# Performance work log

Hardware: AMD Instinct MI355X
Metric: run time of the kernel (lower is better)

Reference implementation:

```python
import jax, jax.numpy as jnp
import numpy as np

B, N, SEQ = 4, 1024, 512
FOUR = SEQ // 2 + 1           # 257, rfft output length
E = N * 32                    # edges from adjacency nonzeros
H1, C1 = 3, 10                # gat1: heads=3, out=10 (concat -> 30)
H2, C2 = 1, 1                 # gat2: heads=1, out=1
NEG_SLOPE = 0.2               # GATConv default negative_slope
PRE_L = 1


def setup_inputs() -> dict:
    ks = jax.random.split(jax.random.key(0), 14)
    occ = jax.random.normal(ks[0], (B, N, SEQ), dtype=jnp.float32)
    prc = jax.random.normal(ks[1], (B, N, SEQ), dtype=jnp.float32)
    # edge_index = adj_dense.nonzero().t(): indices in [0, N)
    edge_index = jax.random.randint(ks[2], (2, E), 0, N, dtype=jnp.int32)
    s = 0.3
    W1 = jax.random.normal(ks[3], (2, H1 * C1), dtype=jnp.float32) * s
    att_src1 = jax.random.normal(ks[4], (1, H1, C1), dtype=jnp.float32) * s
    att_dst1 = jax.random.normal(ks[5], (1, H1, C1), dtype=jnp.float32) * s
    b1 = jnp.zeros((H1 * C1,), dtype=jnp.float32)
    W2 = jax.random.normal(ks[6], (H1 * C1, H2 * C2), dtype=jnp.float32) * s
    att_src2 = jax.random.normal(ks[7], (1, H2, C2), dtype=jnp.float32) * s
    att_dst2 = jax.random.normal(ks[8], (1, H2, C2), dtype=jnp.float32) * s
    b2 = jnp.zeros((H2 * C2,), dtype=jnp.float32)
    dec_W = jax.random.normal(ks[9], (FOUR, PRE_L), dtype=jnp.float32) * (1.0 / np.sqrt(FOUR))
    dec_b = jnp.zeros((PRE_L,), dtype=jnp.float32)
    return {"occ": occ, "prc": prc, "edge_index": edge_index,
            "W1": W1, "att_src1": att_src1, "att_dst1": att_dst1, "b1": b1,
            "W2": W2, "att_src2": att_src2, "att_dst2": att_dst2, "b2": b2,
            "dec_W": dec_W, "dec_b": dec_b}


def gat_layer(x, src, dst, W, att_src, att_dst, bias, heads, ch):
    # x: [Nt, Fin]. PyG GATConv (concat=True, eval mode: no dropout).
    Nt = x.shape[0]
    h = (x @ W).reshape(Nt, heads, ch)                 # [Nt, H, C]
    a_src = jnp.sum(h * att_src, axis=-1)              # [Nt, H]
    a_dst = jnp.sum(h * att_dst, axis=-1)              # [Nt, H]
    e = jax.nn.leaky_relu(a_src[src] + a_dst[dst], NEG_SLOPE)  # [Ee, H]
    # segment softmax over destination nodes
    m = jax.ops.segment_max(e, dst, num_segments=Nt)   # [Nt, H]
    ex = jnp.exp(e - m[dst])
    denom = jax.ops.segment_sum(ex, dst, num_segments=Nt)
    alpha = ex / denom[dst]                            # [Ee, H]
    out = jax.ops.segment_sum(h[src] * alpha[..., None], dst, num_segments=Nt)
    return out.reshape(Nt, heads * ch) + bias


def reference(occ, prc, edge_index, W1, att_src1, att_dst1, b1,
              W2, att_src2, att_dst2, b2, dec_W, dec_b):
    # stack -> [B, N, SEQ, 2]; rfft over seq dim; keep real part
    x = jnp.stack([occ, prc], axis=-1)
    x = jnp.fft.rfft(x, axis=2).real                   # [B, N, FOUR, 2]
    x = x.reshape(-1, 2)                               # [Nt, 2], Nt = B*N*FOUR
    Nt = x.shape[0]
    # GATConv adds self-loops for every row of x (num_nodes = Nt)
    loops = jnp.arange(Nt, dtype=edge_index.dtype)
    src = jnp.concatenate([edge_index[0], loops])
    dst = jnp.concatenate([edge_index[1], loops])
    x = gat_layer(x, src, dst, W1, att_src1, att_dst1, b1, H1, C1)  # [Nt, 30]
    x = jax.nn.elu(x)
    x = gat_layer(x, src, dst, W2, att_src2, att_dst2, b2, H2, C2)  # [Nt, 1]
    # dropout is identity in eval mode
    x = x.reshape(B, N, FOUR)
    return x @ dec_W + dec_b                           # [B, N, PRE_L]
```

## Files before the change

### kernel.cpp

```cpp
#include <hip/hip_runtime.h>
#include <math.h>

constexpr int Bc    = 4;
constexpr int Nc    = 1024;
constexpr int SEQc  = 512;
constexpr int FOURc = 257;
constexpr int NROWS = Bc * Nc;
constexpr int NSMALL = 1024;
constexpr int F1c   = 30;
constexpr int CAP   = 128;
constexpr int XPAD  = 258;
constexpr float NEG_SLOPE = 0.2f;

#define DEVFN static __device__ __forceinline__

__global__ __launch_bounds__(256) void k_xf(
    const float* __restrict__ occ, const float* __restrict__ prc,
    float* __restrict__ xf, int* __restrict__ cnt) {
  __shared__ float4 z[2][128];
  __shared__ float sp[2][6];
  const int tid  = threadIdx.x;
  const int lane = tid & 63;
  const int wid  = tid >> 6;
  const int jrow = wid >> 1;
  const int half = wid & 1;
  const int row  = blockIdx.x * 2 + jrow;

  if (blockIdx.x == 0) {
#pragma unroll
    for (int j = 0; j < 4; ++j) cnt[tid + 256 * j] = 0;
  }

  {
    const int j = tid >> 7;
    const int t = tid & 127;
    const float* ro = occ + (size_t)(blockIdx.x * 2 + j) * SEQc;
    const float* rp = prc + (size_t)(blockIdx.x * 2 + j) * SEQc;
    if (t == 0) {
      sp[j][0] = ro[0];                 sp[j][1] = rp[0];
      sp[j][2] = ro[128] + ro[384];     sp[j][3] = rp[128] + rp[384];
      sp[j][4] = ro[256];               sp[j][5] = rp[256];
    } else {
      float ao = ro[t] + ro[SEQc - t];
      float bo = ro[256 - t] + ro[256 + t];
      float ap = rp[t] + rp[SEQc - t];
      float bp = rp[256 - t] + rp[256 + t];
      z[j][t] = make_float4(ao + bo, ap + bp, ao - bo, ap - bp);
    }
  }
  __syncthreads();

  const int k0 = half * 128 + 2 * lane;
  const float a = 6.283185307179586f / 512.0f;
  float ce = cosf((float)k0 * a),       cpe = 1.f, m2e = 2.f * ce;
  float co = cosf((float)(k0 + 1) * a), cpo = 1.f, m2o = 2.f * co;
  float aeo = 0.f, aep = 0.f, aoo = 0.f, aop = 0.f;

#pragma unroll 4
  for (int t = 1; t < 128; ++t) {
    float4 zv = z[jrow][t];
    aeo = fmaf(zv.x, ce, aeo);
    aep = fmaf(zv.y, ce, aep);
    aoo = fmaf(zv.z, co, aoo);
    aop = fmaf(zv.w, co, aop);
    float ne = fmaf(m2e, ce, -cpe); cpe = ce; ce = ne;
    float no = fmaf(m2o, co, -cpo); cpo = co; co = no;
  }

  const float y0o = sp[jrow][0], y0p = sp[jrow][1];
  const float y128o = sp[jrow][2], y128p = sp[jrow][3];
  const float x256o = sp[jrow][4], x256p = sp[jrow][5];
  const float s128 = (lane & 1) ? -1.f : 1.f;

  float4 st;
  st.x = aeo + y0o + s128 * y128o + x256o;
  st.y = aep + y0p + s128 * y128p + x256p;
  st.z = aoo + y0o - x256o;
  st.w = aop + y0p - x256p;
  *reinterpret_cast<float4*>(xf + ((size_t)row * XPAD + k0) * 2) = st;

  if (half == 0) {
    float sgn = (lane & 1) ? -1.f : 1.f;
    float4 zhi = z[jrow][lane + 64];
    float so = sgn * zhi.x, spp = sgn * zhi.y;
    if (lane >= 1) {
      float4 zlo = z[jrow][lane];
      so  = fmaf(sgn, zlo.x, so);
      spp = fmaf(sgn, zlo.y, spp);
    }
#pragma unroll
    for (int off = 32; off; off >>= 1) {
      so  += __shfl_xor(so, off);
      spp += __shfl_xor(spp, off);
    }
    if (lane == 0) {
      float2 st2;
      st2.x = y0o + y128o + so + x256o;
      st2.y = y0p + y128p + spp + x256p;
      *reinterpret_cast<float2*>(xf + ((size_t)row * XPAD + 256) * 2) = st2;
    }
  }
}

__global__ __launch_bounds__(256) void k_pre(const int* __restrict__ ei, int E,
                                             int* __restrict__ cnt,
                                             int* __restrict__ srcs2) {
  const int base = blockIdx.x * 256 + threadIdx.x;
  const int tot  = E + NSMALL;
  for (int e = base; e < tot; e += 32 * 256) {
    int src, dst;
    if (e < E) { src = ei[e]; dst = ei[E + e]; }
    else       { src = dst = e - E; }
    int pos = atomicAdd(&cnt[dst], 1);
    if (pos < CAP) srcs2[dst * CAP + pos] = src;
  }
}

DEVFN float node_v(float xo, float xp,
                   const float* w1s, const float* b1s, const float* w2s, float b2v) {
  float s = 0.f;
#pragma unroll
  for (int jj = 0; jj < F1c; ++jj) {
    float h = fmaf(xo, w1s[jj], fmaf(xp, w1s[F1c + jj], b1s[jj]));
    float e = h > 0.f ? h : (__expf(h) - 1.f);
    s = fmaf(e, w2s[jj], s);
  }
  return s + b2v;
}

DEVFN void small_prep(int node, float xo, float xp,
                      const float* w1s, const float* s1, const float* d1,
                      float* h1s, float* a1s, float* a1d) {
#pragma unroll
  for (int h = 0; h < 3; ++h) {
    float as = 0.f, ad = 0.f;
#pragma unroll
    for (int c = 0; c < 10; ++c) {
      int jj = h * 10 + c;
      float hv = fmaf(xo, w1s[jj], xp * w1s[F1c + jj]);
      h1s[node * F1c + jj] = hv;
      as = fmaf(hv, s1[jj], as);
      ad = fmaf(hv, d1[jj], ad);
    }
    a1s[node * 3 + h] = as;
    a1d[node * 3 + h] = ad;
  }
}

__global__ __launch_bounds__(256) void k_post(
    const float* __restrict__ xf,
    const float* __restrict__ W1, const float* __restrict__ b1,
    const float* __restrict__ W2, const float* __restrict__ b2,
    const float* __restrict__ as1, const float* __restrict__ ad1,
    const float* __restrict__ decW, const float* __restrict__ decb,
    float* __restrict__ out, float* __restrict__ vsm,
    float* __restrict__ h1s, float* __restrict__ a1s, float* __restrict__ a1d) {
  __shared__ float wl[192];
  __shared__ float red[4];
  const int tid = threadIdx.x;
  const int row = blockIdx.x;
  if      (tid < 60)  wl[tid] = W1[tid];
  else if (tid < 90)  wl[tid] = b1[tid - 60];
  else if (tid < 120) wl[tid] = W2[tid - 90];
  else if (tid < 150) wl[tid] = as1[tid - 120];
  else if (tid < 180) wl[tid] = ad1[tid - 150];
  __syncthreads();
  const float* w1s = wl;
  const float* b1s = wl + 60;
  const float* w2s = wl + 90;
  const float* s1  = wl + 120;
  const float* d1  = wl + 150;
  const float b2v  = b2[0];
  const bool smallrow = (row < 4);

  float2 v2 = *reinterpret_cast<const float2*>(xf + ((size_t)row * XPAD + tid) * 2);
  float vv = node_v(v2.x, v2.y, w1s, b1s, w2s, b2v);
  float s = vv * decW[tid];
  if (tid == 0) {
    float2 v6 = *reinterpret_cast<const float2*>(xf + ((size_t)row * XPAD + 256) * 2);
    float v256 = node_v(v6.x, v6.y, w1s, b1s, w2s, b2v);
    s = fmaf(v256, decW[256], s);
    if (smallrow) {
      int node = row * FOURc + 256;
      if (node < NSMALL) {
        vsm[node] = v256;
        small_prep(node, v6.x, v6.y, w1s, s1, d1, h1s, a1s, a1d);
      }
    }
  }
  if (smallrow) {
    int node = row * FOURc + tid;
    if (node < NSMALL) {
      vsm[node] = vv;
      small_prep(node, v2.x, v2.y, w1s, s1, d1, h1s, a1s, a1d);
    }
  }
#pragma unroll
  for (int off = 32; off; off >>= 1) s += __shfl_xor(s, off);
  if ((tid & 63) == 0) red[tid >> 6] = s;
  __syncthreads();
  if (tid == 0) out[row] = red[0] + red[1] + red[2] + red[3] + decb[0];
}

__global__ __launch_bounds__(256) void k_g1(
    const int* __restrict__ cnt, const int* __restrict__ srcs2,
    const float* __restrict__ a1s, const float* __restrict__ a1d,
    const float* __restrict__ h1s,
    const float* __restrict__ b1, const float* __restrict__ W2,
    const float* __restrict__ as2, const float* __restrict__ ad2,
    float* __restrict__ h2s, float* __restrict__ a2s, float* __restrict__ a2d) {
  const int lane = threadIdx.x & 63;
  const int dst  = blockIdx.x * 4 + (threadIdx.x >> 6);
  const int deg  = cnt[dst];
  const int* sp  = srcs2 + dst * CAP;
  const float ad0 = a1d[dst * 3], ad1v = a1d[dst * 3 + 1], ad2v = a1d[dst * 3 + 2];
  float den[3] = {0.f, 0.f, 0.f};
  float num[F1c];
#pragma unroll
  for (int j = 0; j < F1c; ++j) num[j] = 0.f;

  for (int p = lane; p < deg; p += 64) {
    int src = sp[p];
    const float* hs = h1s + src * F1c;
    float x0 = a1s[src * 3]     + ad0;
    float x1 = a1s[src * 3 + 1] + ad1v;
    float x2 = a1s[src * 3 + 2] + ad2v;
    x0 = x0 > 0.f ? x0 : NEG_SLOPE * x0;
    x1 = x1 > 0.f ? x1 : NEG_SLOPE * x1;
    x2 = x2 > 0.f ? x2 : NEG_SLOPE * x2;
    float e0 = __expf(x0), e1 = __expf(x1), e2 = __expf(x2);
    den[0] += e0; den[1] += e1; den[2] += e2;
#pragma unroll
    for (int c = 0; c < 10; ++c) {
      num[c]      = fmaf(e0, hs[c],      num[c]);
      num[10 + c] = fmaf(e1, hs[10 + c], num[10 + c]);
      num[20 + c] = fmaf(e2, hs[20 + c], num[20 + c]);
    }
  }
#pragma unroll
  for (int h = 0; h < 3; ++h)
#pragma unroll
    for (int off = 32; off; off >>= 1) den[h] += __shfl_xor(den[h], off);
#pragma unroll
  for (int j = 0; j < F1c; ++j)
#pragma unroll
    for (int off = 32; off; off >>= 1) num[j] += __shfl_xor(num[j], off);

  if (lane == 0) {
    float h2 = 0.f;
#pragma unroll
    for (int jj = 0; jj < F1c; ++jj) {
      float x2 = num[jj] / den[jj / 10] + b1[jj];
      x2 = x2 > 0.f ? x2 : (__expf(x2) - 1.f);
      h2 = fmaf(x2, W2[jj], h2);
    }
    h2s[dst] = h2;
    a2s[dst] = h2 * as2[0];
    a2d[dst] = h2 * ad2[0];
  }
}

__global__ __launch_bounds__(256) void k_g2(
    const int* __restrict__ cnt, const int* __restrict__ srcs2,
    const float* __restrict__ a2s, const float* __restrict__ a2d,
    const float* __restrict__ h2s, const float* __restrict__ b2,
    float* __restrict__ val2) {
  const int lane = threadIdx.x & 63;
  const int dst  = blockIdx.x * 4 + (threadIdx.x >> 6);
  const int deg  = cnt[dst];
  const int* sp  = srcs2 + dst * CAP;
  const float adv = a2d[dst];
  float den = 0.f, num = 0.f;
  for (int p = lane; p < deg; p += 64) {
    int src = sp[p];
    float x = a2s[src] + adv;
    x = x > 0.f ? x : NEG_SLOPE * x;
    float ex = __expf(x);
    den += ex;
    num = fmaf(ex, h2s[src], num);
  }
#pragma unroll
  for (int off = 32; off; off >>= 1) {
    den += __shfl_xor(den, off);
    num += __shfl_xor(num, off);
  }
  if (lane == 0) val2[dst] = num / den + b2[0];
}

__global__ __launch_bounds__(256) void k_tail(
    const float* __restrict__ val2, const float* __restrict__ vsm,
    const float* __restrict__ decW, float* __restrict__ out) {
  const int lane = threadIdx.x & 63;
  const int r    = threadIdx.x >> 6;
  float c = 0.f;
  for (int k = lane; k < FOURc; k += 64) {
    int node = r * FOURc + k;
    if (node < NSMALL) c += (val2[node] - vsm[node]) * decW[k];
  }
#pragma unroll
  for (int off = 32; off; off >>= 1) c += __shfl_xor(c, off);
  if (lane == 0) out[r] += c;
}

extern "C" void kernel_launch(void* const* d_in, const int* in_sizes, int n_in,
                              void* d_out, int out_size, void* d_ws, size_t ws_size,
                              hipStream_t stream) {
  const float* occ  = (const float*)d_in[0];
  const float* prc  = (const float*)d_in[1];
  const int*   ei   = (const int*)d_in[2];
  const float* W1   = (const float*)d_in[3];
  const float* as1  = (const float*)d_in[4];
  const float* ad1  = (const float*)d_in[5];
  const float* b1   = (const float*)d_in[6];
  const float* W2   = (const float*)d_in[7];
  const float* as2  = (const float*)d_in[8];
  const float* ad2  = (const float*)d_in[9];
  const float* b2   = (const float*)d_in[10];
  const float* decW = (const float*)d_in[11];
  const float* decb = (const float*)d_in[12];
  const int E = in_sizes[2] / 2;

  float* ws = (float*)d_ws;
  float* xf   = ws;
  float* h1s  = xf + (size_t)NROWS * XPAD * 2;
  float* a1s  = h1s + NSMALL * F1c;
  float* a1d  = a1s + NSMALL * 3;
  float* h2s  = a1d + NSMALL * 3;
  float* a2s  = h2s + NSMALL;
  float* a2d  = a2s + NSMALL;
  float* val2 = a2d + NSMALL;
  float* vsm  = val2 + NSMALL;
  int*   cnt  = (int*)(vsm + NSMALL);
  int*   srcs2 = cnt + NSMALL;

  k_xf<<<NROWS / 2, 256, 0, stream>>>(occ, prc, xf, cnt);

  k_pre<<<32, 256, 0, stream>>>(ei, E, cnt, srcs2);

  k_post<<<NROWS, 256, 0, stream>>>(xf, W1, b1, W2, b2, as1, ad1,
                                    decW, decb, (float*)d_out, vsm,
                                    h1s, a1s, a1d);

  k_g1<<<NSMALL / 4, 256, 0, stream>>>(cnt, srcs2, a1s, a1d, h1s,
                                       b1, W2, as2, ad2, h2s, a2s, a2d);
  k_g2<<<NSMALL / 4, 256, 0, stream>>>(cnt, srcs2, a2s, a2d, h2s, b2, val2);

  k_tail<<<1, 256, 0, stream>>>(val2, vsm, decW, (float*)d_out);
}
```

Before: 56.95 us.

## Fuse rfft and post-GAT stages in shared memory, fold tail into g2

```diff
diff --git a/kernel.cpp b/kernel.cpp
--- a/kernel.cpp
+++ b/kernel.cpp
@@ -9,22 +9,61 @@
 constexpr int NSMALL = 1024;
 constexpr int F1c   = 30;
 constexpr int CAP   = 128;
-constexpr int XPAD  = 258;
+constexpr int XROW  = 520;
 constexpr float NEG_SLOPE = 0.2f;
 
 #define DEVFN static __device__ __forceinline__
 
-__global__ __launch_bounds__(256) void k_xf(
+DEVFN float node_v(float xo, float xp,
+                   const float* w1s, const float* b1s, const float* w2s, float b2v) {
+  float s = 0.f;
+#pragma unroll
+  for (int jj = 0; jj < F1c; ++jj) {
+    float h = fmaf(xo, w1s[jj], fmaf(xp, w1s[F1c + jj], b1s[jj]));
+    float e = h > 0.f ? h : (__expf(h) - 1.f);
+    s = fmaf(e, w2s[jj], s);
+  }
+  return s + b2v;
+}
+
+DEVFN void small_prep(int node, float xo, float xp,
+                      const float* w1s, const float* s1, const float* d1,
+                      float* h1s, float* a1s, float* a1d) {
+#pragma unroll
+  for (int h = 0; h < 3; ++h) {
+    float as = 0.f, ad = 0.f;
+#pragma unroll
+    for (int c = 0; c < 10; ++c) {
+      int jj = h * 10 + c;
+      float hv = fmaf(xo, w1s[jj], xp * w1s[F1c + jj]);
+      h1s[node * F1c + jj] = hv;
+      as = fmaf(hv, s1[jj], as);
+      ad = fmaf(hv, d1[jj], ad);
+    }
+    a1s[node * 3 + h] = as;
+    a1d[node * 3 + h] = ad;
+  }
+}
+
+__global__ __launch_bounds__(256) void k_main(
     const float* __restrict__ occ, const float* __restrict__ prc,
-    float* __restrict__ xf, int* __restrict__ cnt) {
+    const float* __restrict__ W1, const float* __restrict__ b1,
+    const float* __restrict__ W2, const float* __restrict__ b2,
+    const float* __restrict__ as1, const float* __restrict__ ad1,
+    const float* __restrict__ decW, const float* __restrict__ decb,
+    float* __restrict__ out, float* __restrict__ vsm,
+    float* __restrict__ h1s, float* __restrict__ a1s, float* __restrict__ a1d,
+    int* __restrict__ cnt) {
   __shared__ float4 z[2][128];
   __shared__ float sp[2][6];
+  __shared__ float xfl[2 * XROW];
+  __shared__ float wl[192];
+  __shared__ float red0[4], red1[4];
   const int tid  = threadIdx.x;
   const int lane = tid & 63;
   const int wid  = tid >> 6;
   const int jrow = wid >> 1;
   const int half = wid & 1;
-  const int row  = blockIdx.x * 2 + jrow;
 
   if (blockIdx.x == 0) {
 #pragma unroll
@@ -48,57 +87,114 @@
       z[j][t] = make_float4(ao + bo, ap + bp, ao - bo, ap - bp);
     }
   }
+  if      (tid < 60)  wl[tid] = W1[tid];
+  else if (tid < 90)  wl[tid] = b1[tid - 60];
+  else if (tid < 120) wl[tid] = W2[tid - 90];
+  else if (tid < 150) wl[tid] = as1[tid - 120];
+  else if (tid < 180) wl[tid] = ad1[tid - 150];
   __syncthreads();
 
-  const int k0 = half * 128 + 2 * lane;
-  const float a = 6.283185307179586f / 512.0f;
-  float ce = cosf((float)k0 * a),       cpe = 1.f, m2e = 2.f * ce;
-  float co = cosf((float)(k0 + 1) * a), cpo = 1.f, m2o = 2.f * co;
-  float aeo = 0.f, aep = 0.f, aoo = 0.f, aop = 0.f;
-
+  {
+    const int k0 = half * 128 + 2 * lane;
+    const float a = 6.283185307179586f / 512.0f;
+    float ce = cosf((float)k0 * a),       cpe = 1.f, m2e = 2.f * ce;
+    float co = cosf((float)(k0 + 1) * a), cpo = 1.f, m2o = 2.f * co;
+    float aeo = 0.f, aep = 0.f, aoo = 0.f, aop = 0.f;
 #pragma unroll 4
-  for (int t = 1; t < 128; ++t) {
-    float4 zv = z[jrow][t];
-    aeo = fmaf(zv.x, ce, aeo);
-    aep = fmaf(zv.y, ce, aep);
-    aoo = fmaf(zv.z, co, aoo);
-    aop = fmaf(zv.w, co, aop);
-    float ne = fmaf(m2e, ce, -cpe); cpe = ce; ce = ne;
-    float no = fmaf(m2o, co, -cpo); cpo = co; co = no;
-  }
-
-  const float y0o = sp[jrow][0], y0p = sp[jrow][1];
-  const float y128o = sp[jrow][2], y128p = sp[jrow][3];
-  const float x256o = sp[jrow][4], x256p = sp[jrow][5];
-  const float s128 = (lane & 1) ? -1.f : 1.f;
-
-  float4 st;
-  st.x = aeo + y0o + s128 * y128o + x256o;
-  st.y = aep + y0p + s128 * y128p + x256p;
-  st.z = aoo + y0o - x256o;
-  st.w = aop + y0p - x256p;
-  *reinterpret_cast<float4*>(xf + ((size_t)row * XPAD + k0) * 2) = st;
-
-  if (half == 0) {
-    float sgn = (lane & 1) ? -1.f : 1.f;
-    float4 zhi = z[jrow][lane + 64];
-    float so = sgn * zhi.x, spp = sgn * zhi.y;
-    if (lane >= 1) {
-      float4 zlo = z[jrow][lane];
-      so  = fmaf(sgn, zlo.x, so);
-      spp = fmaf(sgn, zlo.y, spp);
-    }
-#pragma unroll
-    for (int off = 32; off; off >>= 1) {
-      so  += __shfl_xor(so, off);
-      spp += __shfl_xor(spp, off);
-    }
-    if (lane == 0) {
-      float2 st2;
-      st2.x = y0o + y128o + so + x256o;
-      st2.y = y0p + y128p + spp + x256p;
-      *reinterpret_cast<float2*>(xf + ((size_t)row * XPAD + 256) * 2) = st2;
-    }
+    for (int t = 1; t < 128; ++t) {
+      float4 zv = z[jrow][t];
+      aeo = fmaf(zv.x, ce, aeo);
+      aep = fmaf(zv.y, ce, aep);
+      aoo = fmaf(zv.z, co, aoo);
+      aop = fmaf(zv.w, co, aop);
+      float ne = fmaf(m2e, ce, -cpe); cpe = ce; ce = ne;
+      float no = fmaf(m2o, co, -cpo); cpo = co; co = no;
+    }
+    const float y0o = sp[jrow][0], y0p = sp[jrow][1];
+    const float y128o = sp[jrow][2], y128p = sp[jrow][3];
+    const float x256o = sp[jrow][4], x256p = sp[jrow][5];
+    const float s128 = (lane & 1) ? -1.f : 1.f;
+
+    float4 st;
+    st.x = aeo + y0o + s128 * y128o + x256o;
+    st.y = aep + y0p + s128 * y128p + x256p;
+    st.z = aoo + y0o - x256o;
+    st.w = aop + y0p - x256p;
+    *reinterpret_cast<float4*>(&xfl[jrow * XROW + k0 * 2]) = st;
+
+    if (half == 0) {
+      float sgn = (lane & 1) ? -1.f : 1.f;
+      float4 zhi = z[jrow][lane + 64];
+      float so = sgn * zhi.x, spp = sgn * zhi.y;
+      if (lane >= 1) {
+        float4 zlo = z[jrow][lane];
+        so  = fmaf(sgn, zlo.x, so);
+        spp = fmaf(sgn, zlo.y, spp);
+      }
+#pragma unroll
+      for (int off = 32; off; off >>= 1) {
+        so  += __shfl_xor(so, off);
+        spp += __shfl_xor(spp, off);
+      }
+      if (lane == 0) {
+        xfl[jrow * XROW + 512] = y0o + y128o + so + x256o;
+        xfl[jrow * XROW + 513] = y0p + y128p + spp + x256p;
+      }
+    }
+  }
+  __syncthreads();
+
+  const float* w1s = wl;
+  const float* b1s = wl + 60;
+  const float* w2s = wl + 90;
+  const float* s1  = wl + 120;
+  const float* d1  = wl + 150;
+  const float b2v  = b2[0];
+  const bool smallblk = (blockIdx.x < 2);
+
+  const float dw = decW[tid];
+  float s0, s1v;
+  {
+    float2 v0 = *reinterpret_cast<const float2*>(&xfl[tid * 2]);
+    float2 v1 = *reinterpret_cast<const float2*>(&xfl[XROW + tid * 2]);
+    float vv0 = node_v(v0.x, v0.y, w1s, b1s, w2s, b2v);
+    float vv1 = node_v(v1.x, v1.y, w1s, b1s, w2s, b2v);
+    s0 = vv0 * dw;
+    s1v = vv1 * dw;
+    if (smallblk) {
+      int row0 = blockIdx.x * 2;
+      int n0 = row0 * FOURc + tid;
+      int n1 = (row0 + 1) * FOURc + tid;
+      if (n0 < NSMALL) { vsm[n0] = vv0; small_prep(n0, v0.x, v0.y, w1s, s1, d1, h1s, a1s, a1d); }
+      if (n1 < NSMALL) { vsm[n1] = vv1; small_prep(n1, v1.x, v1.y, w1s, s1, d1, h1s, a1s, a1d); }
+    }
+  }
+  if (tid == 0) {
+    const float dw6 = decW[256];
+#pragma unroll
+    for (int jr = 0; jr < 2; ++jr) {
+      float xo = xfl[jr * XROW + 512], xp = xfl[jr * XROW + 513];
+      float v256 = node_v(xo, xp, w1s, b1s, w2s, b2v);
+      if (jr == 0) s0 = fmaf(v256, dw6, s0); else s1v = fmaf(v256, dw6, s1v);
+      if (smallblk) {
+        int node = (blockIdx.x * 2 + jr) * FOURc + 256;
+        if (node < NSMALL) {
+          vsm[node] = v256;
+          small_prep(node, xo, xp, w1s, s1, d1, h1s, a1s, a1d);
+        }
+      }
+    }
+  }
+#pragma unroll
+  for (int off = 32; off; off >>= 1) {
+    s0  += __shfl_xor(s0, off);
+    s1v += __shfl_xor(s1v, off);
+  }
+  if (lane == 0) { red0[wid] = s0; red1[wid] = s1v; }
+  __syncthreads();
+  if (tid < 2) {
+    const float* r = tid ? red1 : red0;
+    out[blockIdx.x * 2 + tid] = r[0] + r[1] + r[2] + r[3] + decb[0];
   }
 }
 
@@ -114,92 +210,6 @@
     int pos = atomicAdd(&cnt[dst], 1);
     if (pos < CAP) srcs2[dst * CAP + pos] = src;
   }
-}
-
-DEVFN float node_v(float xo, float xp,
-                   const float* w1s, const float* b1s, const float* w2s, float b2v) {
-  float s = 0.f;
-#pragma unroll
-  for (int jj = 0; jj < F1c; ++jj) {
-    float h = fmaf(xo, w1s[jj], fmaf(xp, w1s[F1c + jj], b1s[jj]));
-    float e = h > 0.f ? h : (__expf(h) - 1.f);
-    s = fmaf(e, w2s[jj], s);
-  }
-  return s + b2v;
-}
-
-DEVFN void small_prep(int node, float xo, float xp,
-                      const float* w1s, const float* s1, const float* d1,
-                      float* h1s, float* a1s, float* a1d) {
-#pragma unroll
-  for (int h = 0; h < 3; ++h) {
-    float as = 0.f, ad = 0.f;
-#pragma unroll
-    for (int c = 0; c < 10; ++c) {
-      int jj = h * 10 + c;
-      float hv = fmaf(xo, w1s[jj], xp * w1s[F1c + jj]);
-      h1s[node * F1c + jj] = hv;
-      as = fmaf(hv, s1[jj], as);
-      ad = fmaf(hv, d1[jj], ad);
-    }
-    a1s[node * 3 + h] = as;
-    a1d[node * 3 + h] = ad;
-  }
-}
-
-__global__ __launch_bounds__(256) void k_post(
-    const float* __restrict__ xf,
-    const float* __restrict__ W1, const float* __restrict__ b1,
-    const float* __restrict__ W2, const float* __restrict__ b2,
-    const float* __restrict__ as1, const float* __restrict__ ad1,
-    const float* __restrict__ decW, const float* __restrict__ decb,
-    float* __restrict__ out, float* __restrict__ vsm,
-    float* __restrict__ h1s, float* __restrict__ a1s, float* __restrict__ a1d) {
-  __shared__ float wl[192];
-  __shared__ float red[4];
-  const int tid = threadIdx.x;
-  const int row = blockIdx.x;
-  if      (tid < 60)  wl[tid] = W1[tid];
-  else if (tid < 90)  wl[tid] = b1[tid - 60];
-  else if (tid < 120) wl[tid] = W2[tid - 90];
-  else if (tid < 150) wl[tid] = as1[tid - 120];
-  else if (tid < 180) wl[tid] = ad1[tid - 150];
-  __syncthreads();
-  const float* w1s = wl;
-  const float* b1s = wl + 60;
-  const float* w2s = wl + 90;
-  const float* s1  = wl + 120;
-  const float* d1  = wl + 150;
-  const float b2v  = b2[0];
-  const bool smallrow = (row < 4);
-
-  float2 v2 = *reinterpret_cast<const float2*>(xf + ((size_t)row * XPAD + tid) * 2);
-  float vv = node_v(v2.x, v2.y, w1s, b1s, w2s, b2v);
-  float s = vv * decW[tid];
-  if (tid == 0) {
-    float2 v6 = *reinterpret_cast<const float2*>(xf + ((size_t)row * XPAD + 256) * 2);
-    float v256 = node_v(v6.x, v6.y, w1s, b1s, w2s, b2v);
-    s = fmaf(v256, decW[256], s);
-    if (smallrow) {
-      int node = row * FOURc + 256;
-      if (node < NSMALL) {
-        vsm[node] = v256;
-        small_prep(node, v6.x, v6.y, w1s, s1, d1, h1s, a1s, a1d);
-      }
-    }
-  }
-  if (smallrow) {
-    int node = row * FOURc + tid;
-    if (node < NSMALL) {
-      vsm[node] = vv;
-      small_prep(node, v2.x, v2.y, w1s, s1, d1, h1s, a1s, a1d);
-    }
-  }
-#pragma unroll
-  for (int off = 32; off; off >>= 1) s += __shfl_xor(s, off);
-  if ((tid & 63) == 0) red[tid >> 6] = s;
-  __syncthreads();
-  if (tid == 0) out[row] = red[0] + red[1] + red[2] + red[3] + decb[0];
 }
 
 __global__ __launch_bounds__(256) void k_g1(
@@ -264,9 +274,14 @@
     const int* __restrict__ cnt, const int* __restrict__ srcs2,
     const float* __restrict__ a2s, const float* __restrict__ a2d,
     const float* __restrict__ h2s, const float* __restrict__ b2,
-    float* __restrict__ val2) {
-  const int lane = threadIdx.x & 63;
-  const int dst  = blockIdx.x * 4 + (threadIdx.x >> 6);
+    const float* __restrict__ vsm, const float* __restrict__ decW,
+    float* __restrict__ out) {
+  __shared__ float rcor[4];
+  __shared__ int   rrow[4];
+  const int tid  = threadIdx.x;
+  const int lane = tid & 63;
+  const int wid  = tid >> 6;
+  const int dst  = blockIdx.x * 4 + wid;
   const int deg  = cnt[dst];
   const int* sp  = srcs2 + dst * CAP;
   const float adv = a2d[dst];
@@ -284,22 +299,23 @@
     den += __shfl_xor(den, off);
     num += __shfl_xor(num, off);
   }
-  if (lane == 0) val2[dst] = num / den + b2[0];
-}
-
-__global__ __launch_bounds__(256) void k_tail(
-    const float* __restrict__ val2, const float* __restrict__ vsm,
-    const float* __restrict__ decW, float* __restrict__ out) {
-  const int lane = threadIdx.x & 63;
-  const int r    = threadIdx.x >> 6;
-  float c = 0.f;
-  for (int k = lane; k < FOURc; k += 64) {
-    int node = r * FOURc + k;
-    if (node < NSMALL) c += (val2[node] - vsm[node]) * decW[k];
-  }
-#pragma unroll
-  for (int off = 32; off; off >>= 1) c += __shfl_xor(c, off);
-  if (lane == 0) out[r] += c;
+  if (lane == 0) {
+    float val2v = num / den + b2[0];
+    int r = dst / FOURc;
+    int k = dst - r * FOURc;
+    rcor[wid] = (val2v - vsm[dst]) * decW[k];
+    rrow[wid] = r;
+  }
+  __syncthreads();
+  if (tid == 0) {
+    float acc = rcor[0];
+#pragma unroll
+    for (int i = 1; i < 4; ++i) {
+      if (rrow[i] == rrow[0]) acc += rcor[i];
+      else atomicAdd(&out[rrow[i]], rcor[i]);
+    }
+    atomicAdd(&out[rrow[0]], acc);
+  }
 }
 
 extern "C" void kernel_launch(void* const* d_in, const int* in_sizes, int n_in,
@@ -321,29 +337,24 @@
   const int E = in_sizes[2] / 2;
 
   float* ws = (float*)d_ws;
-  float* xf   = ws;
-  float* h1s  = xf + (size_t)NROWS * XPAD * 2;
+  float* h1s  = ws;
   float* a1s  = h1s + NSMALL * F1c;
   float* a1d  = a1s + NSMALL * 3;
   float* h2s  = a1d + NSMALL * 3;
   float* a2s  = h2s + NSMALL;
   float* a2d  = a2s + NSMALL;
-  float* val2 = a2d + NSMALL;
-  float* vsm  = val2 + NSMALL;
+  float* vsm  = a2d + NSMALL;
   int*   cnt  = (int*)(vsm + NSMALL);
   int*   srcs2 = cnt + NSMALL;
 
-  k_xf<<<NROWS / 2, 256, 0, stream>>>(occ, prc, xf, cnt);
+  k_main<<<NROWS / 2, 256, 0, stream>>>(occ, prc, W1, b1, W2, b2, as1, ad1,
+                                        decW, decb, (float*)d_out, vsm,
+                                        h1s, a1s, a1d, cnt);
 
   k_pre<<<32, 256, 0, stream>>>(ei, E, cnt, srcs2);
-
-  k_post<<<NROWS, 256, 0, stream>>>(xf, W1, b1, W2, b2, as1, ad1,
-                                    decW, decb, (float*)d_out, vsm,
-                                    h1s, a1s, a1d);
 
   k_g1<<<NSMALL / 4, 256, 0, stream>>>(cnt, srcs2, a1s, a1d, h1s,
                                        b1, W2, as2, ad2, h2s, a2s, a2d);
-  k_g2<<<NSMALL / 4, 256, 0, stream>>>(cnt, srcs2, a2s, a2d, h2s, b2, val2);
-
-  k_tail<<<1, 256, 0, stream>>>(val2, vsm, decW, (float*)d_out);
-}
+  k_g2<<<NSMALL / 4, 256, 0, stream>>>(cnt, srcs2, a2s, a2d, h2s, b2,
+                                       vsm, decW, (float*)d_out);
+}
```

After: 67.10 us. +17.8%, slower.
